# Performance work log

Measured on AMD Instinct MI355X. Metric: run time of the kernel, lower is better.

The kernel has to match this reference:

```python
import jax, jax.numpy as jnp
import numpy as np

B, S, D_IN, D = 8, 4096, 512, 256


def setup_inputs() -> dict:
    key = jax.random.key(0)
    ks = jax.random.split(key, 7)
    s_in = 1.0 / np.sqrt(D_IN)
    return {
        "x": jax.random.normal(ks[0], (B, S, D_IN), dtype=jnp.float32),
        "Wq": jax.random.normal(ks[1], (D_IN, D), dtype=jnp.float32) * s_in,
        "bq": jnp.zeros((D,), dtype=jnp.float32),
        "Wk": jax.random.normal(ks[2], (D_IN, D), dtype=jnp.float32) * s_in,
        "bk": jnp.zeros((D,), dtype=jnp.float32),
        "Wv": jax.random.normal(ks[3], (D_IN, D), dtype=jnp.float32) * s_in,
        "bv": jnp.zeros((D,), dtype=jnp.float32),
    }


def reference(x, Wq, bq, Wk, bk, Wv, bv):
    # Q/K/V projections (three Dense layers in the original)
    Q = jnp.einsum("bsd,de->bse", x, Wq) + bq  # [B,S,D]
    K = jnp.einsum("bsd,de->bse", x, Wk) + bk
    V = jnp.einsum("bsd,de->bse", x, Wv) + bv
    # scaled dot-product attention: softmax(QK^T / sqrt(d)) V
    scale = 1.0 / jnp.sqrt(jnp.asarray(Q.shape[-1], dtype=Q.dtype))
    scores = jnp.einsum("bqe,bke->bqk", Q, K) * scale  # [B,S,S]
    attn = jax.nn.softmax(scores, axis=-1)
    out = jnp.einsum("bqk,bke->bqe", attn, V)  # [B,S,D]
    return out
```

## Files before the change

kernel.cpp:

```cpp
#include <hip/hip_runtime.h>
#include <hip/hip_bf16.h>
#include <stdint.h>

#define B_   8
#define S_   4096
#define DIN  512
#define D_   256
#define ROWS (B_ * S_)

typedef __attribute__((ext_vector_type(8))) short short8;
typedef __attribute__((ext_vector_type(4))) float floatx4;
typedef __attribute__((ext_vector_type(16))) float floatx16;
typedef __attribute__((ext_vector_type(4))) short short4v;
typedef __attribute__((ext_vector_type(2))) unsigned uint2v;

__device__ __forceinline__ void gll16(const void* g, void* lds) {
  __builtin_amdgcn_global_load_lds(
      (const __attribute__((address_space(1))) void*)g,
      (__attribute__((address_space(3))) void*)lds, 16, 0, 0);
}
__device__ __forceinline__ short f2bf(float x) {
  union { float f; unsigned u; } c; c.f = x;
  unsigned r = (c.u + 0x7FFF + ((c.u >> 16) & 1)) >> 16;
  return (short)r;
}
__device__ __forceinline__ float bf2f(short v) {
  union { unsigned u; float f; } c; c.u = ((unsigned)(unsigned short)v) << 16;
  return c.f;
}
__device__ __forceinline__ unsigned pk2bf(float a, float b) {
  union { __hip_bfloat162 h; unsigned u; } c;
  c.h = __float22bfloat162_rn(float2{a, b});
  return c.u;
}
__device__ __forceinline__ float fexp2(float x) {
#if __has_builtin(__builtin_amdgcn_exp2f)
  return __builtin_amdgcn_exp2f(x);
#else
  return exp2f(x);
#endif
}

__device__ __forceinline__ void plswap(unsigned& a, unsigned& b, int H) {
#if __has_builtin(__builtin_amdgcn_permlane32_swap)
  uint2v r = __builtin_amdgcn_permlane32_swap(a, b, false, false);
  a = r[0]; b = r[1];
#else
  unsigned sa = (unsigned)__shfl_xor((int)a, 32);
  unsigned sb = (unsigned)__shfl_xor((int)b, 32);
  unsigned na = H ? sb : a;
  unsigned nb = H ? b : sa;
  a = na; b = nb;
#endif
}

__device__ __forceinline__ float halfsum(float x) {
#if __has_builtin(__builtin_amdgcn_permlane32_swap)
  union { float f; unsigned u; } c; c.f = x;
  uint2v r = __builtin_amdgcn_permlane32_swap(c.u, c.u, false, false);
  union { unsigned u; float f; } a, b; a.u = r[0]; b.u = r[1];
  return a.f + b.f;
#else
  return x + __shfl_xor(x, 32);
#endif
}

__global__ __launch_bounds__(256) void detect_kernel(
    const unsigned short* __restrict__ w, int* __restrict__ flag) {
  const int tid = threadIdx.x;
  float m = 0.f;
#pragma unroll
  for (int j = 0; j < 16; ++j) {
    float f = bf2f((short)w[tid * 16 + j]);
    m = fmaxf(m, fabsf(f));
  }
#pragma unroll
  for (int d = 1; d < 64; d <<= 1) m = fmaxf(m, __shfl_xor(m, d));
  __shared__ float red[4];
  if ((tid & 63) == 0) red[tid >> 6] = m;
  __syncthreads();
  if (tid == 0) {
    float mm = fmaxf(fmaxf(red[0], red[1]), fmaxf(red[2], red[3]));
    flag[0] = (mm > 1000.0f) ? 1 : 0;
  }
}

__global__ __launch_bounds__(256) void cvt_kernel(
    const void* __restrict__ src, short* __restrict__ dst, int n,
    const int* __restrict__ flag) {
  const int i = blockIdx.x * 256 + threadIdx.x;
  if (i * 8 >= n) return;
  if (*flag) {
    float4 a = ((const float4*)src)[2 * i];
    float4 b = ((const float4*)src)[2 * i + 1];
    short8 o;
    o[0] = f2bf(a.x); o[1] = f2bf(a.y); o[2] = f2bf(a.z); o[3] = f2bf(a.w);
    o[4] = f2bf(b.x); o[5] = f2bf(b.y); o[6] = f2bf(b.z); o[7] = f2bf(b.w);
    ((short8*)dst)[i] = o;
  } else {
    ((short8*)dst)[i] = ((const short8*)src)[i];
  }
}

__global__ __launch_bounds__(256) void wtcvt_kernel(
    const void* __restrict__ Wq, const void* __restrict__ Wk,
    const void* __restrict__ Wv, short* __restrict__ Wt,
    const int* __restrict__ flag) {
  __shared__ float tile[32][33];
  const int mat = blockIdx.z;
  const void* W = (mat == 0) ? Wq : ((mat == 1) ? Wk : Wv);
  const int n0 = blockIdx.x * 32, k0 = blockIdx.y * 32;
  const int tx = threadIdx.x & 31, ty = threadIdx.x >> 5;
  const bool f32 = (*flag != 0);
#pragma unroll
  for (int i = 0; i < 4; ++i) {
    int k = ty + i * 8;
    float v = f32 ? ((const float*)W)[(k0 + k) * D_ + n0 + tx]
                  : bf2f(((const short*)W)[(k0 + k) * D_ + n0 + tx]);
    tile[k][tx] = v;
  }
  __syncthreads();
  short* o = Wt + mat * (D_ * DIN);
#pragma unroll
  for (int i = 0; i < 4; ++i) {
    int n = ty + i * 8;
    o[(n0 + n) * DIN + k0 + tx] = f2bf(tile[tx][n]);
  }
}

__global__ __launch_bounds__(256) void biascvt_kernel(
    const void* __restrict__ bq, const void* __restrict__ bk,
    const void* __restrict__ bv, short* __restrict__ bbuf,
    const int* __restrict__ flag) {
  const int tid = threadIdx.x;
  const bool f32 = (*flag != 0);
  const void* p[3] = {bq, bk, bv};
#pragma unroll
  for (int m = 0; m < 3; ++m)
    bbuf[m * D_ + tid] = f32 ? f2bf(((const float*)p[m])[tid])
                             : ((const short*)p[m])[tid];
}

__global__ __launch_bounds__(256, 2) void qkv_kernel(
    const short* __restrict__ x, const short* __restrict__ Wt,
    const short* __restrict__ bb,
    short* __restrict__ Qg, short* __restrict__ Kg, short* __restrict__ Vtg) {
  __shared__ short As[2][512 * 8];
  __shared__ short Bs[2][512 * 8];
  const int tid = threadIdx.x;
  const int lane = tid & 63, w = tid >> 6;
  const int li = lane & 15, g = lane >> 4;
  const int mb = blockIdx.x;
  const int mat = blockIdx.y >> 1, nb = blockIdx.y & 1;
  const short* Ag = x + mb * 128 * DIN;
  const short* Bt = Wt + mat * (D_ * DIN) + nb * 128 * DIN;

  auto stage = [&](int buf, int k0) {
#pragma unroll
    for (int p = 0; p < 2; ++p) {
      int c = p * 256 + tid;
      int row = c >> 2, og = (c & 3) ^ (row & 3);
      gll16(Ag + row * DIN + k0 + og * 8, &As[buf][(p * 256 + w * 64) * 8]);
    }
#pragma unroll
    for (int p = 0; p < 2; ++p) {
      int c = p * 256 + tid;
      int row = c >> 2, og = (c & 3) ^ (row & 3);
      gll16(Bt + row * DIN + k0 + og * 8, &Bs[buf][(p * 256 + w * 64) * 8]);
    }
  };

  const int msub = (w & 1) * 64, nsub = (w >> 1) * 64;
  floatx4 acc[4][4];
#pragma unroll
  for (int i = 0; i < 4; ++i)
#pragma unroll
    for (int j = 0; j < 4; ++j) acc[i][j] = floatx4{0.f, 0.f, 0.f, 0.f};

  stage(0, 0);
  __syncthreads();
  for (int kt = 0; kt < 16; ++kt) {
    if (kt < 15) stage((kt + 1) & 1, (kt + 1) * 32);
    const int buf = kt & 1;
    short8 af[4], bfr[4];
#pragma unroll
    for (int mt = 0; mt < 4; ++mt) {
      int row = msub + mt * 16 + li;
      int og = g ^ (row & 3);
      af[mt] = *(const short8*)&As[buf][(row * 4 + og) * 8];
    }
#pragma unroll
    for (int nt = 0; nt < 4; ++nt) {
      int row = nsub + nt * 16 + li;
      int og = g ^ (row & 3);
      bfr[nt] = *(const short8*)&Bs[buf][(row * 4 + og) * 8];
    }
#pragma unroll
    for (int mt = 0; mt < 4; ++mt)
#pragma unroll
      for (int nt = 0; nt < 4; ++nt)
        acc[mt][nt] = __builtin_amdgcn_mfma_f32_16x16x32_bf16(
            af[mt], bfr[nt], acc[mt][nt], 0, 0, 0);
    __syncthreads();
  }

  const short* bias = bb + mat * 256;
  if (mat < 2) {
    short* O = (mat == 0) ? Qg : Kg;
#pragma unroll
    for (int nt = 0; nt < 4; ++nt) {
      float bv_ = bf2f(bias[nb * 128 + nsub + nt * 16 + li]);
#pragma unroll
      for (int mt = 0; mt < 4; ++mt)
#pragma unroll
        for (int r = 0; r < 4; ++r) {
          int m = mb * 128 + msub + mt * 16 + g * 4 + r;
          int n = nb * 128 + nsub + nt * 16 + li;
          O[m * D_ + n] = f2bf(acc[mt][nt][r] + bv_);
        }
    }
  } else {
#pragma unroll
    for (int nt = 0; nt < 4; ++nt) {
      float bv_ = bf2f(bias[nb * 128 + nsub + nt * 16 + li]);
#pragma unroll
      for (int mt = 0; mt < 4; ++mt) {
        int m0 = mb * 128 + msub + mt * 16 + g * 4;
        int batch = m0 >> 12, s = m0 & (S_ - 1);
        int n = nb * 128 + nsub + nt * 16 + li;
        short4v pk;
#pragma unroll
        for (int r = 0; r < 4; ++r) pk[r] = f2bf(acc[mt][nt][r] + bv_);
        *(short4v*)&Vtg[(batch * D_ + n) * S_ + s] = pk;
      }
    }
  }
}

__global__ __launch_bounds__(256, 2) void attn_kernel(
    const short* __restrict__ Qg, const short* __restrict__ Kg,
    const short* __restrict__ Vtg, short* __restrict__ Op,
    float* __restrict__ lsum) {
  extern __shared__ short smem[];
  short* Ksb = smem;
  short* Vsb = smem + 16384;
  const int tid = threadIdx.x, lane = tid & 63, w = tid >> 6;
  const int q = lane & 31, H = lane >> 5;
  const int id = blockIdx.x;
  const int bb = id & 7;
  const int h = (id >> 3) & 1;
  const int q0 = (id >> 4) * 128;
  const int qrow = q0 + w * 32;
  const int s_base = h * 2048;
  const int l8 = lane * 8;

  const short* Qb = Qg + (size_t)(bb * S_ + qrow) * D_;
  const short* Kb = Kg + (size_t)bb * S_ * D_;
  const short* Vb = Vtg + (size_t)bb * D_ * S_;

  short8 qf[16];
#pragma unroll
  for (int o = 0; o < 16; ++o)
    qf[o] = *(const short8*)&Qb[q * D_ + o * 16 + H * 8];

  floatx16 oa[8];
#pragma unroll
  for (int n2 = 0; n2 < 8; ++n2)
#pragma unroll
    for (int i = 0; i < 16; ++i) oa[n2][i] = 0.f;
  float lst = 0.f;

  auto stageK = [&](int t, short* kdst) {
    const int s0 = s_base + t * 32;
#pragma unroll
    for (int p = 0; p < 4; ++p) {
      int c = p * 256 + tid;
      int oct = c >> 5, s = c & 31;
      gll16(&Kb[(s0 + s) * D_ + oct * 8], &kdst[c * 8]);
    }
  };
  auto stageV = [&](int t, short* vdst) {
    const int s0 = s_base + t * 32;
#pragma unroll
    for (int p = 0; p < 4; ++p) {
      int c = p * 256 + tid;
      int e = (c >> 7) * 32 + (c & 31), oct = (c >> 5) & 3;
      gll16(&Vb[e * S_ + s0 + oct * 8], &vdst[c * 8]);
    }
  };

  const float cs = 0.09016844005556f;
  const float M12 = 12.0f;

  stageK(0, Ksb);
  stageV(0, Vsb);
  __syncthreads();

  short8 pA, pB;

  {
    stageK(1, Ksb + 8192);
    stageV(1, Vsb + 8192);
    floatx16 sc;
#pragma unroll
    for (int i = 0; i < 16; ++i) sc[i] = 0.f;
    __builtin_amdgcn_s_setprio(1);
#pragma unroll
    for (int o = 0; o < 16; ++o) {
      short8 kf = *(const short8*)&Ksb[l8 + o * 512];
      sc = __builtin_amdgcn_mfma_f32_32x32x16_bf16(kf, qf[o], sc, 0, 0, 0);
    }
    __builtin_amdgcn_s_setprio(0);
    unsigned dw[8];
    float rs = 0.f;
#pragma unroll
    for (int i = 0; i < 16; i += 2) {
      float a = fexp2(sc[i] * cs - M12);
      float b = fexp2(sc[i + 1] * cs - M12);
      dw[i >> 1] = pk2bf(a, b);
      rs += a + b;
    }
    plswap(dw[0], dw[2], H); plswap(dw[1], dw[3], H);
    plswap(dw[4], dw[6], H); plswap(dw[5], dw[7], H);
    union { unsigned u[4]; short8 s; } ka, kb2;
    ka.u[0] = dw[0]; ka.u[1] = dw[1]; ka.u[2] = dw[2]; ka.u[3] = dw[3];
    kb2.u[0] = dw[4]; kb2.u[1] = dw[5]; kb2.u[2] = dw[6]; kb2.u[3] = dw[7];
    pA = ka.s; pB = kb2.s;
    lst += halfsum(rs);
    __syncthreads();
  }

  int vst = 2, vrd = 0;
  for (int t = 1; t < 64; ++t) {
    if (t < 63) {
      stageK(t + 1, Ksb + (((t + 1) & 1) ? 8192 : 0));
      stageV(t + 1, Vsb + vst * 8192);
    }
    const short* Kr = Ksb + ((t & 1) ? 8192 : 0);
    const short* Vr = Vsb + vrd * 8192;

    floatx16 sc;
#pragma unroll
    for (int i = 0; i < 16; ++i) sc[i] = 0.f;
    __builtin_amdgcn_s_setprio(1);
#pragma unroll
    for (int o = 0; o < 16; ++o) {
      short8 kf = *(const short8*)&Kr[l8 + o * 512];
      sc = __builtin_amdgcn_mfma_f32_32x32x16_bf16(kf, qf[o], sc, 0, 0, 0);
      const int n2 = o & 7;
      short8 vf = *(const short8*)&Vr[l8 + (n2 * 2 + (o >> 3)) * 512];
      oa[n2] = __builtin_amdgcn_mfma_f32_32x32x16_bf16(
          vf, (o < 8) ? pA : pB, oa[n2], 0, 0, 0);
    }
    __builtin_amdgcn_s_setprio(0);

    unsigned dw[8];
    float rs = 0.f;
#pragma unroll
    for (int i = 0; i < 16; i += 2) {
      float a = fexp2(sc[i] * cs - M12);
      float b = fexp2(sc[i + 1] * cs - M12);
      dw[i >> 1] = pk2bf(a, b);
      rs += a + b;
    }
    plswap(dw[0], dw[2], H); plswap(dw[1], dw[3], H);
    plswap(dw[4], dw[6], H); plswap(dw[5], dw[7], H);
    union { unsigned u[4]; short8 s; } ka, kb2;
    ka.u[0] = dw[0]; ka.u[1] = dw[1]; ka.u[2] = dw[2]; ka.u[3] = dw[3];
    kb2.u[0] = dw[4]; kb2.u[1] = dw[5]; kb2.u[2] = dw[6]; kb2.u[3] = dw[7];
    pA = ka.s; pB = kb2.s;
    lst += halfsum(rs);

    vst = (vst == 2) ? 0 : vst + 1;
    vrd = (vrd == 2) ? 0 : vrd + 1;
    __syncthreads();
  }

  {
    const short* Vr = Vsb + vrd * 8192;
    __builtin_amdgcn_s_setprio(1);
#pragma unroll
    for (int o = 0; o < 16; ++o) {
      const int n2 = o & 7;
      short8 vf = *(const short8*)&Vr[l8 + (n2 * 2 + (o >> 3)) * 512];
      oa[n2] = __builtin_amdgcn_mfma_f32_32x32x16_bf16(
          vf, (o < 8) ? pA : pB, oa[n2], 0, 0, 0);
    }
    __builtin_amdgcn_s_setprio(0);
  }

  const float inv = 1.0f / lst;
  short* Oh = Op + (size_t)h * ROWS * D_ + (size_t)(bb * S_ + qrow) * D_;
#pragma unroll
  for (int n2 = 0; n2 < 8; ++n2) {
#pragma unroll
    for (int qd = 0; qd < 4; ++qd) {
      int e0 = n2 * 32 + 8 * qd + 4 * H;
      uint2v st;
      st[0] = pk2bf(oa[n2][4 * qd] * inv, oa[n2][4 * qd + 1] * inv);
      st[1] = pk2bf(oa[n2][4 * qd + 2] * inv, oa[n2][4 * qd + 3] * inv);
      *(uint2v*)&Oh[q * D_ + e0] = st;
    }
  }
  if (H == 0) {
    int grow = bb * S_ + qrow + q;
    lsum[h * ROWS + grow] = lst;
  }
}

__global__ __launch_bounds__(256) void combine_kernel(
    const short* __restrict__ Op, const float* __restrict__ lsum,
    void* __restrict__ outv, const int* __restrict__ flag) {
  const int gid = blockIdx.x * 256 + threadIdx.x;
  const int row = gid >> 6;
  const int e4 = (gid & 63) * 4;
  const float l1 = lsum[row], l2 = lsum[ROWS + row];
  const float inv = 1.0f / (l1 + l2);
  const float c1 = l1 * inv, c2 = l2 * inv;
  short4v a = *(const short4v*)&Op[(size_t)row * D_ + e4];
  short4v b = *(const short4v*)&Op[(size_t)(ROWS + row) * D_ + e4];
  if (*flag) {
    float4 o;
    o.x = c1 * bf2f(a[0]) + c2 * bf2f(b[0]);
    o.y = c1 * bf2f(a[1]) + c2 * bf2f(b[1]);
    o.z = c1 * bf2f(a[2]) + c2 * bf2f(b[2]);
    o.w = c1 * bf2f(a[3]) + c2 * bf2f(b[3]);
    *(float4*)&((float*)outv)[(size_t)row * D_ + e4] = o;
  } else {
    short4v o;
#pragma unroll
    for (int j = 0; j < 4; ++j)
      o[j] = f2bf(c1 * bf2f(a[j]) + c2 * bf2f(b[j]));
    *(short4v*)&((short*)outv)[(size_t)row * D_ + e4] = o;
  }
}

extern "C" void kernel_launch(void* const* d_in, const int* in_sizes, int n_in,
                              void* d_out, int out_size, void* d_ws, size_t ws_size,
                              hipStream_t stream) {
  const void* x  = d_in[0];
  const void* Wq = d_in[1];
  const void* bq = d_in[2];
  const void* Wk = d_in[3];
  const void* bk = d_in[4];
  const void* Wv = d_in[5];
  const void* bv = d_in[6];
  char* ws = (char*)d_ws;
  int*   flag = (int*)(ws);
  short* bbuf = (short*)(ws + 256);
  float* lsum = (float*)(ws + 4096);
  short* Wt   = (short*)(ws + (1u << 20));
  short* xb   = (short*)(ws + (2u << 20));
  short* Qw   = (short*)(ws + (34u << 20));
  short* Kw   = (short*)(ws + (50u << 20));
  short* Vtw  = (short*)(ws + (66u << 20));
  short* Op   = xb;

  hipLaunchKernelGGL(detect_kernel, dim3(1), dim3(256), 0, stream,
                     (const unsigned short*)Wq, flag);
  hipLaunchKernelGGL(cvt_kernel, dim3(8192), dim3(256), 0, stream,
                     x, xb, B_ * S_ * DIN, flag);
  hipLaunchKernelGGL(wtcvt_kernel, dim3(8, 16, 3), dim3(256), 0, stream,
                     Wq, Wk, Wv, Wt, flag);
  hipLaunchKernelGGL(biascvt_kernel, dim3(1), dim3(256), 0, stream,
                     bq, bk, bv, bbuf, flag);
  hipLaunchKernelGGL(qkv_kernel, dim3(256, 6), dim3(256), 0, stream,
                     xb, Wt, bbuf, Qw, Kw, Vtw);
  hipLaunchKernelGGL(attn_kernel, dim3(512), dim3(256), 81920, stream,
                     Qw, Kw, Vtw, Op, lsum);
  hipLaunchKernelGGL(combine_kernel, dim3(ROWS / 4), dim3(256), 0, stream,
                     Op, lsum, d_out, flag);
}
```

Measured before the change: 326.5 us.

## Fuse x fp32-to-bf16 conversion into QKV GEMM staging and merge bias conversion

After: 318.8 us. -2.4%, faster.

```diff
diff --git a/kernel.cpp b/kernel.cpp
--- a/kernel.cpp
+++ b/kernel.cpp
@@ -85,26 +85,11 @@
   }
 }
 
-__global__ __launch_bounds__(256) void cvt_kernel(
-    const void* __restrict__ src, short* __restrict__ dst, int n,
-    const int* __restrict__ flag) {
-  const int i = blockIdx.x * 256 + threadIdx.x;
-  if (i * 8 >= n) return;
-  if (*flag) {
-    float4 a = ((const float4*)src)[2 * i];
-    float4 b = ((const float4*)src)[2 * i + 1];
-    short8 o;
-    o[0] = f2bf(a.x); o[1] = f2bf(a.y); o[2] = f2bf(a.z); o[3] = f2bf(a.w);
-    o[4] = f2bf(b.x); o[5] = f2bf(b.y); o[6] = f2bf(b.z); o[7] = f2bf(b.w);
-    ((short8*)dst)[i] = o;
-  } else {
-    ((short8*)dst)[i] = ((const short8*)src)[i];
-  }
-}
-
 __global__ __launch_bounds__(256) void wtcvt_kernel(
     const void* __restrict__ Wq, const void* __restrict__ Wk,
     const void* __restrict__ Wv, short* __restrict__ Wt,
+    const void* __restrict__ bq, const void* __restrict__ bk,
+    const void* __restrict__ bv, short* __restrict__ bbuf,
     const int* __restrict__ flag) {
   __shared__ float tile[32][33];
   const int mat = blockIdx.z;
@@ -119,6 +104,12 @@
                   : bf2f(((const short*)W)[(k0 + k) * D_ + n0 + tx]);
     tile[k][tx] = v;
   }
+  if (blockIdx.x == 0 && blockIdx.y == 0) {
+    const void* bp = (mat == 0) ? bq : ((mat == 1) ? bk : bv);
+    bbuf[mat * D_ + threadIdx.x] =
+        f32 ? f2bf(((const float*)bp)[threadIdx.x])
+            : ((const short*)bp)[threadIdx.x];
+  }
   __syncthreads();
   short* o = Wt + mat * (D_ * DIN);
 #pragma unroll
@@ -128,22 +119,9 @@
   }
 }
 
-__global__ __launch_bounds__(256) void biascvt_kernel(
-    const void* __restrict__ bq, const void* __restrict__ bk,
-    const void* __restrict__ bv, short* __restrict__ bbuf,
-    const int* __restrict__ flag) {
-  const int tid = threadIdx.x;
-  const bool f32 = (*flag != 0);
-  const void* p[3] = {bq, bk, bv};
-#pragma unroll
-  for (int m = 0; m < 3; ++m)
-    bbuf[m * D_ + tid] = f32 ? f2bf(((const float*)p[m])[tid])
-                             : ((const short*)p[m])[tid];
-}
-
 __global__ __launch_bounds__(256, 2) void qkv_kernel(
-    const short* __restrict__ x, const short* __restrict__ Wt,
-    const short* __restrict__ bb,
+    const void* __restrict__ xin, const short* __restrict__ Wt,
+    const short* __restrict__ bb, const int* __restrict__ flag,
     short* __restrict__ Qg, short* __restrict__ Kg, short* __restrict__ Vtg) {
   __shared__ short As[2][512 * 8];
   __shared__ short Bs[2][512 * 8];
@@ -152,16 +130,14 @@
   const int li = lane & 15, g = lane >> 4;
   const int mb = blockIdx.x;
   const int mat = blockIdx.y >> 1, nb = blockIdx.y & 1;
-  const short* Ag = x + mb * 128 * DIN;
+  const bool f32 = (*flag != 0);
+  const short* Ag = (const short*)xin + (size_t)mb * 128 * DIN;
+  const float* Af = (const float*)xin + (size_t)mb * 128 * DIN;
   const short* Bt = Wt + mat * (D_ * DIN) + nb * 128 * DIN;
 
-  auto stage = [&](int buf, int k0) {
-#pragma unroll
-    for (int p = 0; p < 2; ++p) {
-      int c = p * 256 + tid;
-      int row = c >> 2, og = (c & 3) ^ (row & 3);
-      gll16(Ag + row * DIN + k0 + og * 8, &As[buf][(p * 256 + w * 64) * 8]);
-    }
+  float4 h0[2], h1[2];
+
+  auto stageB = [&](int buf, int k0) {
 #pragma unroll
     for (int p = 0; p < 2; ++p) {
       int c = p * 256 + tid;
@@ -169,6 +145,40 @@
       gll16(Bt + row * DIN + k0 + og * 8, &Bs[buf][(p * 256 + w * 64) * 8]);
     }
   };
+  auto stageA_issue = [&](int buf, int k0) {
+    if (f32) {
+#pragma unroll
+      for (int p = 0; p < 2; ++p) {
+        int c = p * 256 + tid;
+        int row = c >> 2, og = (c & 3) ^ (row & 3);
+        const float4* src =
+            (const float4*)(Af + (size_t)row * DIN + k0 + og * 8);
+        h0[p] = src[0];
+        h1[p] = src[1];
+      }
+    } else {
+#pragma unroll
+      for (int p = 0; p < 2; ++p) {
+        int c = p * 256 + tid;
+        int row = c >> 2, og = (c & 3) ^ (row & 3);
+        gll16(Ag + row * DIN + k0 + og * 8, &As[buf][(p * 256 + w * 64) * 8]);
+      }
+    }
+  };
+  auto stageA_write = [&](int buf) {
+    if (f32) {
+#pragma unroll
+      for (int p = 0; p < 2; ++p) {
+        int c = p * 256 + tid;
+        short8 o;
+        o[0] = f2bf(h0[p].x); o[1] = f2bf(h0[p].y);
+        o[2] = f2bf(h0[p].z); o[3] = f2bf(h0[p].w);
+        o[4] = f2bf(h1[p].x); o[5] = f2bf(h1[p].y);
+        o[6] = f2bf(h1[p].z); o[7] = f2bf(h1[p].w);
+        *(short8*)&As[buf][c * 8] = o;
+      }
+    }
+  };
 
   const int msub = (w & 1) * 64, nsub = (w >> 1) * 64;
   floatx4 acc[4][4];
@@ -177,10 +187,16 @@
 #pragma unroll
     for (int j = 0; j < 4; ++j) acc[i][j] = floatx4{0.f, 0.f, 0.f, 0.f};
 
-  stage(0, 0);
+  stageB(0, 0);
+  stageA_issue(0, 0);
+  stageA_write(0);
   __syncthreads();
   for (int kt = 0; kt < 16; ++kt) {
-    if (kt < 15) stage((kt + 1) & 1, (kt + 1) * 32);
+    const int nbuf = (kt + 1) & 1;
+    if (kt < 15) {
+      stageB(nbuf, (kt + 1) * 32);
+      stageA_issue(nbuf, (kt + 1) * 32);
+    }
     const int buf = kt & 1;
     short8 af[4], bfr[4];
 #pragma unroll
@@ -201,6 +217,7 @@
       for (int nt = 0; nt < 4; ++nt)
         acc[mt][nt] = __builtin_amdgcn_mfma_f32_16x16x32_bf16(
             af[mt], bfr[nt], acc[mt][nt], 0, 0, 0);
+    if (kt < 15) stageA_write(nbuf);
     __syncthreads();
   }
 
@@ -412,26 +429,32 @@
     const short* __restrict__ Op, const float* __restrict__ lsum,
     void* __restrict__ outv, const int* __restrict__ flag) {
   const int gid = blockIdx.x * 256 + threadIdx.x;
-  const int row = gid >> 6;
-  const int e4 = (gid & 63) * 4;
+  const int row = gid >> 5;
+  const int e8 = (gid & 31) * 8;
   const float l1 = lsum[row], l2 = lsum[ROWS + row];
   const float inv = 1.0f / (l1 + l2);
   const float c1 = l1 * inv, c2 = l2 * inv;
-  short4v a = *(const short4v*)&Op[(size_t)row * D_ + e4];
-  short4v b = *(const short4v*)&Op[(size_t)(ROWS + row) * D_ + e4];
+  short8 a = *(const short8*)&Op[(size_t)row * D_ + e8];
+  short8 b = *(const short8*)&Op[(size_t)(ROWS + row) * D_ + e8];
   if (*flag) {
-    float4 o;
-    o.x = c1 * bf2f(a[0]) + c2 * bf2f(b[0]);
-    o.y = c1 * bf2f(a[1]) + c2 * bf2f(b[1]);
-    o.z = c1 * bf2f(a[2]) + c2 * bf2f(b[2]);
-    o.w = c1 * bf2f(a[3]) + c2 * bf2f(b[3]);
-    *(float4*)&((float*)outv)[(size_t)row * D_ + e4] = o;
+    float4 o0, o1;
+    o0.x = c1 * bf2f(a[0]) + c2 * bf2f(b[0]);
+    o0.y = c1 * bf2f(a[1]) + c2 * bf2f(b[1]);
+    o0.z = c1 * bf2f(a[2]) + c2 * bf2f(b[2]);
+    o0.w = c1 * bf2f(a[3]) + c2 * bf2f(b[3]);
+    o1.x = c1 * bf2f(a[4]) + c2 * bf2f(b[4]);
+    o1.y = c1 * bf2f(a[5]) + c2 * bf2f(b[5]);
+    o1.z = c1 * bf2f(a[6]) + c2 * bf2f(b[6]);
+    o1.w = c1 * bf2f(a[7]) + c2 * bf2f(b[7]);
+    float* dst = (float*)outv + (size_t)row * D_ + e8;
+    *(float4*)dst = o0;
+    *(float4*)(dst + 4) = o1;
   } else {
-    short4v o;
-#pragma unroll
-    for (int j = 0; j < 4; ++j)
+    short8 o;
+#pragma unroll
+    for (int j = 0; j < 8; ++j)
       o[j] = f2bf(c1 * bf2f(a[j]) + c2 * bf2f(b[j]));
-    *(short4v*)&((short*)outv)[(size_t)row * D_ + e4] = o;
+    *(short8*)&((short*)outv)[(size_t)row * D_ + e8] = o;
   }
 }
 
@@ -450,24 +473,19 @@
   short* bbuf = (short*)(ws + 256);
   float* lsum = (float*)(ws + 4096);
   short* Wt   = (short*)(ws + (1u << 20));
-  short* xb   = (short*)(ws + (2u << 20));
+  short* Op   = (short*)(ws + (2u << 20));
   short* Qw   = (short*)(ws + (34u << 20));
   short* Kw   = (short*)(ws + (50u << 20));
   short* Vtw  = (short*)(ws + (66u << 20));
-  short* Op   = xb;
 
   hipLaunchKernelGGL(detect_kernel, dim3(1), dim3(256), 0, stream,
                      (const unsigned short*)Wq, flag);
-  hipLaunchKernelGGL(cvt_kernel, dim3(8192), dim3(256), 0, stream,
-                     x, xb, B_ * S_ * DIN, flag);
   hipLaunchKernelGGL(wtcvt_kernel, dim3(8, 16, 3), dim3(256), 0, stream,
-                     Wq, Wk, Wv, Wt, flag);
-  hipLaunchKernelGGL(biascvt_kernel, dim3(1), dim3(256), 0, stream,
-                     bq, bk, bv, bbuf, flag);
+                     Wq, Wk, Wv, Wt, bq, bk, bv, bbuf, flag);
   hipLaunchKernelGGL(qkv_kernel, dim3(256, 6), dim3(256), 0, stream,
-                     xb, Wt, bbuf, Qw, Kw, Vtw);
+                     x, Wt, bbuf, flag, Qw, Kw, Vtw);
   hipLaunchKernelGGL(attn_kernel, dim3(512), dim3(256), 81920, stream,
                      Qw, Kw, Vtw, Op, lsum);
-  hipLaunchKernelGGL(combine_kernel, dim3(ROWS / 4), dim3(256), 0, stream,
+  hipLaunchKernelGGL(combine_kernel, dim3(ROWS / 8), dim3(256), 0, stream,
                      Op, lsum, d_out, flag);
 }
```
